# Kernel optimization log

Hardware: AMD Instinct MI355X
Metric: run time of the kernel (lower is better)

The kernel has to match this reference:

```python
import jax, jax.numpy as jnp
import numpy as np

N = 50000
E = 800000
IN_C = 128
OUT_C = 64   # per-head dim C == out_channels (concat=False)
HEADS = 4
FFN_H = 256
SQRT_HALF = 0.70710678
LN_EPS = 1e-7


def setup_inputs() -> dict:
    key = jax.random.key(0)
    ks = jax.random.split(key, 16)
    s = 0.05
    return {
        "x": jax.random.normal(ks[0], (N, IN_C), jnp.float32),
        "edge_index": jax.random.randint(ks[1], (2, E), 0, N, jnp.int64),
        # GATv2 params
        "Wl": jax.random.normal(ks[2], (HEADS * OUT_C, IN_C), jnp.float32) * s,
        "Wr": jax.random.normal(ks[3], (HEADS * OUT_C, IN_C), jnp.float32) * s,
        "att": jax.random.normal(ks[4], (HEADS, OUT_C), jnp.float32) * s,
        "bias": jax.random.normal(ks[5], (OUT_C,), jnp.float32) * s,
        # block linears
        "W_affn1": jax.random.normal(ks[6], (OUT_C, IN_C), jnp.float32) * s,
        "b_affn1": jnp.zeros((OUT_C,), jnp.float32),
        "W_affn2": jax.random.normal(ks[7], (OUT_C, OUT_C), jnp.float32) * s,
        "b_affn2": jnp.zeros((OUT_C,), jnp.float32),
        # layernorms
        "g1": jnp.ones((IN_C,), jnp.float32),
        "beta1": jnp.zeros((IN_C,), jnp.float32),
        "g2": jnp.ones((OUT_C,), jnp.float32),
        "beta2": jnp.zeros((OUT_C,), jnp.float32),
        # FFN: out_channels -> 256 -> out_channels
        "W1": jax.random.normal(ks[8], (FFN_H, OUT_C), jnp.float32) * s,
        "b1": jnp.zeros((FFN_H,), jnp.float32),
        "W2": jax.random.normal(ks[9], (OUT_C, FFN_H), jnp.float32) * s,
        "b2": jnp.zeros((OUT_C,), jnp.float32),
    }


def _ln(v, g, b):
    m = jnp.mean(v, axis=-1, keepdims=True)
    var = jnp.var(v, axis=-1, keepdims=True)
    return (v - m) * jax.lax.rsqrt(var + LN_EPS) * g + b


def reference(x, edge_index, Wl, Wr, att, bias, W_affn1, b_affn1,
              W_affn2, b_affn2, g1, beta1, g2, beta2, W1, b1, W2, b2):
    n = x.shape[0]
    H, C = att.shape
    dst = edge_index[0]
    src = edge_index[1]

    x_res = x @ W_affn1.T + b_affn1            # (N, OUT_C)
    h = _ln(x, g1, beta1)                      # (N, IN_C)

    # GATv2 attention (concat=False, no self loops)
    x_l = (h @ Wl.T).reshape(n, H, C)
    x_r = (h @ Wr.T).reshape(n, H, C)
    x_j = x_r[src]                             # (E, H, C)
    e = jax.nn.leaky_relu(x_l[dst] + x_j, 0.2) # (E, H, C)
    logits = jnp.einsum('ehc,hc->eh', e, att)  # (E, H)

    # segment softmax over destination nodes (per head)
    mx = jax.ops.segment_max(logits, dst, num_segments=n)
    ex = jnp.exp(logits - mx[dst])
    den = jax.ops.segment_sum(ex, dst, num_segments=n)
    alpha = ex / (den[dst] + 1e-16)            # (E, H)

    agg = jnp.zeros((n, H, C), x.dtype).at[dst].add(x_j * alpha[..., None])
    attn_out = jnp.mean(agg, axis=1) + bias    # (N, OUT_C)

    out = SQRT_HALF * attn_out + SQRT_HALF * x_res

    # FFN half of the block (pre-LN, matching the attention half's structure)
    h2 = _ln(out, g2, beta2)
    f = jax.nn.relu(h2 @ W1.T + b1) @ W2.T + b2
    res2 = out @ W_affn2.T + b_affn2
    return SQRT_HALF * f + SQRT_HALF * res2
```

## Files before the change

### kernel.cpp

```cpp
#include <hip/hip_runtime.h>
#include <hip/hip_bf16.h>
#include <hip/hip_fp16.h>
#include <math.h>


#define SQRT_HALF 0.70710678f
#define LN_EPS 1e-7f

typedef __attribute__((ext_vector_type(8))) short bf16x8;
typedef __attribute__((ext_vector_type(4))) float f32x4;
typedef _Float16 f16x2 __attribute__((ext_vector_type(2)));

__device__ __forceinline__ float wave_reduce_sum64(float v) {
  #pragma unroll
  for (int m = 1; m < 64; m <<= 1) v += __shfl_xor(v, m, 64);
  return v;
}
__device__ __forceinline__ unsigned short f2bf_bits(float f) {
  __hip_bfloat16 b = __float2bfloat16(f);
  return *reinterpret_cast<unsigned short*>(&b);
}
__device__ __forceinline__ unsigned int pack2bf(float lo, float hi) {
  return (unsigned int)f2bf_bits(lo) | ((unsigned int)f2bf_bits(hi) << 16);
}
__device__ __forceinline__ __half2 u2h(unsigned int u) {
  union { unsigned int u; __half2 h; } c; c.u = u; return c.h;
}
__device__ __forceinline__ __half2 h2abs(__half2 v) {
  union { __half2 h; unsigned int u; } c; c.h = v;
  c.u &= 0x7fff7fffu;
  return c.h;
}
__device__ __forceinline__ f16x2 h2f(__half2 h) {
  union { __half2 h; f16x2 f; } c; c.h = h; return c.f;
}
__device__ __forceinline__ __half2 shflx_h2(__half2 v, int m) {
  union { unsigned int u; __half2 h; } c; c.h = v;
  c.u = (unsigned int)__shfl_xor((int)c.u, m, 64);
  return c.h;
}
__device__ __forceinline__ float dpp_xor1_add(float p) {
  int t = __builtin_amdgcn_update_dpp(0, __float_as_int(p), 0xB1, 0xf, 0xf, true);
  return p + __int_as_float(t);
}
__device__ __forceinline__ float dpp_xor2_add(float p) {
  int t = __builtin_amdgcn_update_dpp(0, __float_as_int(p), 0x4E, 0xf, 0xf, true);
  return p + __int_as_float(t);
}
__device__ __forceinline__ bf16x8 cvt8(float4 a0, float4 a1) {
  bf16x8 v;
  v[0] = (short)f2bf_bits(a0.x); v[1] = (short)f2bf_bits(a0.y);
  v[2] = (short)f2bf_bits(a0.z); v[3] = (short)f2bf_bits(a0.w);
  v[4] = (short)f2bf_bits(a1.x); v[5] = (short)f2bf_bits(a1.y);
  v[6] = (short)f2bf_bits(a1.z); v[7] = (short)f2bf_bits(a1.w);
  return v;
}

#define NCHUNK 128
#define SBUK 4608

__global__ __launch_bounds__(256) void prep_kernel(
    const float* __restrict__ x, const float* __restrict__ g1,
    const float* __restrict__ beta1, __hip_bfloat16* __restrict__ h,
    const float* __restrict__ wl, const float* __restrict__ wr,
    const float* __restrict__ wa1, const float* __restrict__ w1,
    const float* __restrict__ w2, const float* __restrict__ wa2,
    const float* __restrict__ b2c, const float* __restrict__ ba2,
    const float* __restrict__ att,
    __hip_bfloat16* __restrict__ wcat, __hip_bfloat16* __restrict__ wa1b,
    __hip_bfloat16* __restrict__ w1b, __hip_bfloat16* __restrict__ w2b,
    __hip_bfloat16* __restrict__ wa2b, __half* __restrict__ att2,
    float* __restrict__ biasc,
    const int* __restrict__ ei, unsigned int* __restrict__ counts,
    int E_, int n, int NBUK, int S, int gLN) {
  __shared__ unsigned int bins[256];
  int bx = blockIdx.x, tid = threadIdx.x;
  if (bx < gLN) {
    int node = bx * 4 + (tid >> 6);
    if (node >= n) return;
    int lane = tid & 63;
    const float* xr = x + (size_t)node * 128;
    float a = xr[lane], c = xr[lane + 64];
    float s1 = wave_reduce_sum64(a + c) * (1.f / 128.f);
    float s2 = wave_reduce_sum64(a * a + c * c) * (1.f / 128.f);
    float inv = rsqrtf(s2 - s1 * s1 + LN_EPS);
    __hip_bfloat16* hr = h + (size_t)node * 128;
    hr[lane]      = __float2bfloat16((a - s1) * inv * g1[lane] + beta1[lane]);
    hr[lane + 64] =
        __float2bfloat16((c - s1) * inv * g1[lane + 64] + beta1[lane + 64]);
  } else if (bx < gLN + NCHUNK) {
    int c = bx - gLN;
    bins[tid] = 0u;
    __syncthreads();
    int e0 = c * S, e1 = c * S + S;
    if (e1 > E_) e1 = E_;
    for (int e = e0 + tid; e < e1; e += 256)
      atomicAdd(&bins[ei[e] >> 8], 1u);
    __syncthreads();
    if (tid < NBUK) counts[(size_t)c * NBUK + tid] = bins[tid];
  } else {
    int gid = (bx - gLN - NCHUNK) * 256 + tid;
    for (int i = gid; i < 110912; i += 64 * 256) {
      if (i < 65536) {
        wcat[i] = __float2bfloat16(i < 32768 ? wl[i] : wr[i - 32768]);
      } else if (i < 73728) {
        int j = i - 65536; wa1b[j] = __float2bfloat16(wa1[j]);
      } else if (i < 90112) {
        int j = i - 73728; w1b[j] = __float2bfloat16(w1[j]);
      } else if (i < 106496) {
        int j = i - 90112; w2b[j] = __float2bfloat16(w2[j]);
      } else if (i < 110592) {
        int j = i - 106496; wa2b[j] = __float2bfloat16(wa2[j]);
      } else if (i < 110848) {
        int j = i - 110592; att2[j] = __float2half(att[j]);
      } else {
        int j = i - 110848; biasc[j] = SQRT_HALF * (b2c[j] + ba2[j]);
      }
    }
  }
}

__global__ __launch_bounds__(256) void scanA_kernel(
    unsigned int* __restrict__ counts, unsigned int* __restrict__ totals,
    int NBUK) {
  int b = blockIdx.x * 4 + (threadIdx.x >> 6);
  if (b >= NBUK) return;
  int lane = threadIdx.x & 63;
  unsigned int a0 = counts[(size_t)(2 * lane) * NBUK + b];
  unsigned int a1 = counts[(size_t)(2 * lane + 1) * NBUK + b];
  unsigned int ps = a0 + a1;
  unsigned int run = ps;
  #pragma unroll
  for (int off = 1; off < 64; off <<= 1) {
    unsigned int u = __shfl_up(run, off, 64);
    if (lane >= off) run += u;
  }
  unsigned int excl = run - ps;
  counts[(size_t)(2 * lane) * NBUK + b] = excl;
  counts[(size_t)(2 * lane + 1) * NBUK + b] = excl + a0;
  if (lane == 63) totals[b] = run;
}

__global__ __launch_bounds__(256) void mfma_pre(
    const short* __restrict__ h, const float* __restrict__ x,
    const short* __restrict__ wcat, const short* __restrict__ wa1b,
    const float* __restrict__ ba1, __half* __restrict__ xlxr,
    float* __restrict__ xres, const int* __restrict__ ei,
    const unsigned int* __restrict__ counts,
    unsigned int* __restrict__ recs,
    int E_, int n, int NBUK, int S, int ntiles) {
  __shared__ unsigned int bins[256];
  int tid = threadIdx.x;
  int wv = tid >> 6, l = tid & 63;
  int lane_m = l & 15, kg = l >> 4;
  if (blockIdx.y < 4) {
    int bn = blockIdx.y * 128;
    bf16x8 wf[4][8];
    const short* wp = wcat + (size_t)(bn + lane_m) * 128 + kg * 8;
    #pragma unroll
    for (int ks = 0; ks < 4; ++ks)
      #pragma unroll
      for (int ct = 0; ct < 8; ++ct)
        wf[ks][ct] = *(const bf16x8*)(wp + (size_t)ct * 16 * 128 + ks * 32);
    for (int t = blockIdx.x; t < ntiles; t += gridDim.x) {
      int node = t * 64 + wv * 16 + lane_m;
      int nodec = node < n ? node : n - 1;
      const short* ap = h + (size_t)nodec * 128 + kg * 8;
      f32x4 acc[8] = {};
      #pragma unroll
      for (int ks = 0; ks < 4; ++ks) {
        bf16x8 af = *(const bf16x8*)(ap + ks * 32);
        #pragma unroll
        for (int ct = 0; ct < 8; ++ct)
          acc[ct] = __builtin_amdgcn_mfma_f32_16x16x32_bf16(
              wf[ks][ct], af, acc[ct], 0, 0, 0);
      }
      if (node < n) {
        #pragma unroll
        for (int ct = 0; ct < 8; ++ct) {
          int col = bn + ct * 16 + kg * 4;
          ushort4 s;
          s.x = __half_as_ushort(__float2half(acc[ct][0]));
          s.y = __half_as_ushort(__float2half(acc[ct][1]));
          s.z = __half_as_ushort(__float2half(acc[ct][2]));
          s.w = __half_as_ushort(__float2half(acc[ct][3]));
          *(ushort4*)((unsigned short*)xlxr + (size_t)node * 512 + col) = s;
        }
      }
    }
  } else if (blockIdx.y == 4) {
    bf16x8 wf[4][4];
    const short* wp = wa1b + (size_t)lane_m * 128 + kg * 8;
    #pragma unroll
    for (int ks = 0; ks < 4; ++ks)
      #pragma unroll
      for (int ct = 0; ct < 4; ++ct)
        wf[ks][ct] = *(const bf16x8*)(wp + (size_t)ct * 16 * 128 + ks * 32);
    float4 bias4[4];
    #pragma unroll
    for (int ct = 0; ct < 4; ++ct)
      bias4[ct] = *(const float4*)(ba1 + ct * 16 + kg * 4);
    for (int t = blockIdx.x; t < ntiles; t += gridDim.x) {
      int node = t * 64 + wv * 16 + lane_m;
      int nodec = node < n ? node : n - 1;
      const float* xrow = x + (size_t)nodec * 128 + kg * 8;
      bf16x8 af[4];
      #pragma unroll
      for (int ks = 0; ks < 4; ++ks) {
        float4 a0 = *(const float4*)(xrow + ks * 32);
        float4 a1 = *(const float4*)(xrow + ks * 32 + 4);
        af[ks] = cvt8(a0, a1);
      }
      f32x4 acc[4] = {};
      #pragma unroll
      for (int ks = 0; ks < 4; ++ks)
        #pragma unroll
        for (int ct = 0; ct < 4; ++ct)
          acc[ct] = __builtin_amdgcn_mfma_f32_16x16x32_bf16(
              wf[ks][ct], af[ks], acc[ct], 0, 0, 0);
      if (node < n) {
        #pragma unroll
        for (int ct = 0; ct < 4; ++ct) {
          int col = ct * 16 + kg * 4;
          *(float4*)(xres + (size_t)node * 64 + col) = make_float4(
              acc[ct][0] + ((const float*)&bias4[ct])[0],
              acc[ct][1] + ((const float*)&bias4[ct])[1],
              acc[ct][2] + ((const float*)&bias4[ct])[2],
              acc[ct][3] + ((const float*)&bias4[ct])[3]);
        }
      }
    }
  } else {
    int c = blockIdx.x;
    if (c >= NCHUNK) return;
    bins[tid] = 0u;
    __syncthreads();
    int e0 = c * S, e1 = c * S + S;
    if (e1 > E_) e1 = E_;
    const unsigned int* cpref = counts + (size_t)c * NBUK;
    for (int e = e0 + tid; e < e1; e += 256) {
      int dst = ei[e], src = ei[E_ + e];
      int b = dst >> 8;
      unsigned int pos = atomicAdd(&bins[b], 1u);
      unsigned int off = (unsigned int)b * SBUK + cpref[b] + pos;
      if (off < (unsigned int)(b + 1) * SBUK)
        recs[off] = ((unsigned int)(dst & 255) << 16) | (unsigned int)src;
    }
  }
}

__global__ __launch_bounds__(512) void bucket_kernel(
    const unsigned int* __restrict__ recs,
    const unsigned int* __restrict__ totals,
    unsigned short* __restrict__ ell, unsigned int* __restrict__ degw,
    int n) {
  __shared__ unsigned int bins[256];
  __shared__ unsigned short ellb[256 * 64];
  int b = blockIdx.x, tid = threadIdx.x;
  if (tid < 256) bins[tid] = 0u;
  __syncthreads();
  unsigned int start = (unsigned int)b * SBUK;
  unsigned int nrec = totals[b];
  for (unsigned int i = tid; i < nrec; i += 512) {
    unsigned int r = recs[start + i];
    int dlow = (int)(r >> 16);
    unsigned int pos = atomicAdd(&bins[dlow], 1u);
    if (pos < 64) ellb[(dlow << 6) + pos] = (unsigned short)(r & 0xffffu);
  }
  __syncthreads();
  if (tid < 256) {
    int d = (int)bins[tid];
    d = d < 64 ? d : 64;
    unsigned short fill = d > 0 ? ellb[(tid << 6) + d - 1] : (unsigned short)0;
    for (int s = d; s < 64; ++s) ellb[(tid << 6) + s] = fill;
  }
  __syncthreads();
  int node0 = b << 8;
  int nn = n - node0;
  nn = nn < 256 ? nn : 256;
  int nquad = nn * 16;
  ushort4* gq = (ushort4*)(ell + ((size_t)node0 << 6));
  const ushort4* lq = (const ushort4*)ellb;
  for (int qd = tid; qd < nquad; qd += 512) gq[qd] = lq[qd];
  int nw = (nn + 3) >> 2;
  for (int w = tid; w < nw; w += 512) {
    unsigned int d0 = bins[4 * w + 0], d1 = bins[4 * w + 1];
    unsigned int d2 = bins[4 * w + 2], d3 = bins[4 * w + 3];
    d0 = d0 < 64u ? d0 : 64u; d1 = d1 < 64u ? d1 : 64u;
    d2 = d2 < 64u ? d2 : 64u; d3 = d3 < 64u ? d3 : 64u;
    degw[(node0 >> 2) + w] = d0 | (d1 << 8) | (d2 << 16) | (d3 << 24);
  }
}

__global__ __launch_bounds__(256) void fused_edge_kernel(
    const unsigned int* __restrict__ degw, const unsigned short* __restrict__ ell,
    const __half* __restrict__ xlxr,
    const __half* __restrict__ att2, const float* __restrict__ xres,
    const float* __restrict__ bias, const float* __restrict__ g2,
    const float* __restrict__ b2, __hip_bfloat16* __restrict__ outb,
    __hip_bfloat16* __restrict__ h2, int n) {
  int node = blockIdx.x * 4 + (threadIdx.x >> 6);
  if (node >= n) return;
  int lane = threadIdx.x & 63;
  int half_ = lane >> 5;
  int hl = lane & 31;
  int q = hl & 7;
  int off8 = (hl >> 3) * 64 + q * 8;
  uint4 va = *(const uint4*)(xlxr + (size_t)node * 512 + off8);
  __half2 xa2[4] = {u2h(va.x), u2h(va.y), u2h(va.z), u2h(va.w)};
  uint4 vt = *(const uint4*)(att2 + off8);
  const __half2 c06 = __float2half2_rn(0.6f);
  const __half2 c04 = __float2half2_rn(0.4f);
  __half2 at6[4], at4[4];
  #pragma unroll
  for (int c = 0; c < 4; ++c) {
    __half2 a = u2h(((const unsigned int*)&vt)[c]);
    at6[c] = __hmul2(c06, a);
    at4[c] = __hmul2(c04, a);
  }
  int d = (int)((degw[node >> 2] >> ((node & 3) * 8)) & 0xffu);
  float den = 0.f;
  __half2 ac2[4] = {__float2half2_rn(0.f), __float2half2_rn(0.f),
                    __float2half2_rn(0.f), __float2half2_rn(0.f)};
  if (d > 0) {
    int dpairs = d >> 1;
    const __half* xrbase = xlxr + 256 + off8;
    int myidx = (int)ell[((size_t)node << 6) + lane];
    int srcA = __shfl(myidx, half_, 64);
    int srcB = __shfl(myidx, 2 + half_, 64);
    uint4 vbA = *(const uint4*)(xrbase + (size_t)srcA * 512);
    uint4 vbB = *(const uint4*)(xrbase + (size_t)srcB * 512);
    #pragma unroll 2
    for (int k = 0; k < dpairs; ++k) {
      int srcC = __shfl(myidx, 2 * k + 4 + half_, 64);
      uint4 vbC = *(const uint4*)(xrbase + (size_t)srcC * 512);
      __half2 xb2[4] = {u2h(vbA.x), u2h(vbA.y), u2h(vbA.z), u2h(vbA.w)};
      float p = 0.f;
      #pragma unroll
      for (int c = 0; c < 4; ++c) {
        __half2 s = __hadd2(xa2[c], xb2[c]);
        p = __builtin_amdgcn_fdot2(h2f(at6[c]), h2f(s), p, false);
        p = __builtin_amdgcn_fdot2(h2f(at4[c]), h2f(h2abs(s)), p, false);
      }
      p = dpp_xor1_add(p);
      p = dpp_xor2_add(p);
      p += __shfl_xor(p, 4, 64);
      float ex = __expf(p);
      den += ex;
      __half2 ex2 = __float2half2_rn(ex);
      #pragma unroll
      for (int c = 0; c < 4; ++c) ac2[c] = __hfma2(ex2, xb2[c], ac2[c]);
      vbA = vbB; vbB = vbC;
    }
    if (d & 1) {
      __half2 xb2[4] = {u2h(vbA.x), u2h(vbA.y), u2h(vbA.z), u2h(vbA.w)};
      float p = 0.f;
      #pragma unroll
      for (int c = 0; c < 4; ++c) {
        __half2 s = __hadd2(xa2[c], xb2[c]);
        p = __builtin_amdgcn_fdot2(h2f(at6[c]), h2f(s), p, false);
        p = __builtin_amdgcn_fdot2(h2f(at4[c]), h2f(h2abs(s)), p, false);
      }
      p = dpp_xor1_add(p);
      p = dpp_xor2_add(p);
      p += __shfl_xor(p, 4, 64);
      float ex = (half_ == 0) ? __expf(p) : 0.f;
      den += ex;
      __half2 ex2 = __float2half2_rn(ex);
      #pragma unroll
      for (int c = 0; c < 4; ++c) ac2[c] = __hfma2(ex2, xb2[c], ac2[c]);
    }
  }
  #pragma unroll
  for (int c = 0; c < 4; ++c) ac2[c] = __hadd2(ac2[c], shflx_h2(ac2[c], 32));
  den += __shfl_xor(den, 32, 64);
  float inv = 1.f / (den + 1e-16f);
  __half2 inv2 = __float2half2_rn(inv);
  #pragma unroll
  for (int c = 0; c < 4; ++c) {
    __half2 a = __hmul2(ac2[c], inv2);
    a = __hadd2(a, shflx_h2(a, 8));
    a = __hadd2(a, shflx_h2(a, 16));
    ac2[c] = a;
  }
  float acf[8];
  #pragma unroll
  for (int c = 0; c < 4; ++c) {
    acf[2 * c]     = __low2float(ac2[c]);
    acf[2 * c + 1] = __high2float(ac2[c]);
  }
  float o[8];
  {
    float4 bi0 = *(const float4*)(bias + q * 8);
    float4 bi1 = *(const float4*)(bias + q * 8 + 4);
    float4 xr0 = *(const float4*)(xres + (size_t)node * 64 + q * 8);
    float4 xr1 = *(const float4*)(xres + (size_t)node * 64 + q * 8 + 4);
    float bi[8] = {bi0.x, bi0.y, bi0.z, bi0.w, bi1.x, bi1.y, bi1.z, bi1.w};
    float xr[8] = {xr0.x, xr0.y, xr0.z, xr0.w, xr1.x, xr1.y, xr1.z, xr1.w};
    #pragma unroll
    for (int c = 0; c < 8; ++c)
      o[c] = SQRT_HALF * (acf[c] * 0.25f + bi[c] + xr[c]);
  }
  float s1 = 0.f, s2 = 0.f;
  #pragma unroll
  for (int c = 0; c < 8; ++c) { s1 += o[c]; s2 += o[c] * o[c]; }
  s1 = dpp_xor1_add(s1); s2 = dpp_xor1_add(s2);
  s1 = dpp_xor2_add(s1); s2 = dpp_xor2_add(s2);
  s1 += __shfl_xor(s1, 4, 64); s2 += __shfl_xor(s2, 4, 64);
  float mean = s1 * (1.f / 64.f);
  float var = s2 * (1.f / 64.f) - mean * mean;
  float rinv = rsqrtf(var + LN_EPS);
  if (lane < 8) {
    float4 g0 = *(const float4*)(g2 + q * 8);
    float4 g1v = *(const float4*)(g2 + q * 8 + 4);
    float4 e0 = *(const float4*)(b2 + q * 8);
    float4 e1 = *(const float4*)(b2 + q * 8 + 4);
    float gg[8] = {g0.x, g0.y, g0.z, g0.w, g1v.x, g1v.y, g1v.z, g1v.w};
    float ee[8] = {e0.x, e0.y, e0.z, e0.w, e1.x, e1.y, e1.z, e1.w};
    uint4 ov, hv;
    ov.x = pack2bf(o[0], o[1]); ov.y = pack2bf(o[2], o[3]);
    ov.z = pack2bf(o[4], o[5]); ov.w = pack2bf(o[6], o[7]);
    float t[8];
    #pragma unroll
    for (int c = 0; c < 8; ++c)
      t[c] = (o[c] - mean) * rinv * gg[c] + ee[c];
    hv.x = pack2bf(t[0], t[1]); hv.y = pack2bf(t[2], t[3]);
    hv.z = pack2bf(t[4], t[5]); hv.w = pack2bf(t[6], t[7]);
    *(uint4*)((unsigned short*)outb + (size_t)node * 64 + q * 8) = ov;
    *(uint4*)((unsigned short*)h2 + (size_t)node * 64 + q * 8) = hv;
  }
}

__global__ __launch_bounds__(256) void ffn_fused(
    const __hip_bfloat16* __restrict__ h2, const __hip_bfloat16* __restrict__ outb,
    const __hip_bfloat16* __restrict__ w1b, const __hip_bfloat16* __restrict__ w2b,
    const __hip_bfloat16* __restrict__ wa2b, const float* __restrict__ b1,
    const float* __restrict__ biasc, float* __restrict__ out,
    int n, int ntiles) {
  __shared__ unsigned short lds[4][16][280];
  int tid = threadIdx.x;
  int wv = tid >> 6, l = tid & 63;
  int lane_m = l & 15, kg = l >> 4;
  bf16x8 wf1[2][16];
  #pragma unroll
  for (int ks = 0; ks < 2; ++ks)
    #pragma unroll
    for (int ct = 0; ct < 16; ++ct)
      wf1[ks][ct] = *(const bf16x8*)(
          (const short*)w1b + (size_t)(ct * 16 + lane_m) * 64 + ks * 32 + kg * 8);
  for (int t = blockIdx.x; t < ntiles; t += gridDim.x) {
    int node = t * 64 + wv * 16 + lane_m;
    int nodec = node < n ? node : n - 1;
    const short* hp = (const short*)h2 + (size_t)nodec * 64 + kg * 8;
    bf16x8 af1[2];
    af1[0] = *(const bf16x8*)(hp);
    af1[1] = *(const bf16x8*)(hp + 32);
    f32x4 acc1[16] = {};
    #pragma unroll
    for (int ks = 0; ks < 2; ++ks)
      #pragma unroll
      for (int ct = 0; ct < 16; ++ct)
        acc1[ct] = __builtin_amdgcn_mfma_f32_16x16x32_bf16(
            wf1[ks][ct], af1[ks], acc1[ct], 0, 0, 0);
    #pragma unroll
    for (int ct = 0; ct < 16; ++ct) {
      float4 bb = *(const float4*)(b1 + ct * 16 + kg * 4);
      ushort4 s;
      s.x = f2bf_bits(fmaxf(acc1[ct][0] + bb.x, 0.f));
      s.y = f2bf_bits(fmaxf(acc1[ct][1] + bb.y, 0.f));
      s.z = f2bf_bits(fmaxf(acc1[ct][2] + bb.z, 0.f));
      s.w = f2bf_bits(fmaxf(acc1[ct][3] + bb.w, 0.f));
      *(ushort4*)&lds[wv][lane_m][ct * 16 + kg * 4] = s;
    }
    f32x4 acc2[4] = {};
    #pragma unroll
    for (int ks = 0; ks < 8; ++ks) {
      bf16x8 af2 = *(const bf16x8*)&lds[wv][lane_m][ks * 32 + kg * 8];
      #pragma unroll
      for (int ct = 0; ct < 4; ++ct) {
        bf16x8 wf2 = *(const bf16x8*)(
            (const short*)w2b + (size_t)(ct * 16 + lane_m) * 256 + ks * 32 + kg * 8);
        acc2[ct] = __builtin_amdgcn_mfma_f32_16x16x32_bf16(
            wf2, af2, acc2[ct], 0, 0, 0);
      }
    }
    const short* op = (const short*)outb + (size_t)nodec * 64 + kg * 8;
    #pragma unroll
    for (int ks = 0; ks < 2; ++ks) {
      bf16x8 afo = *(const bf16x8*)(op + ks * 32);
      #pragma unroll
      for (int ct = 0; ct < 4; ++ct) {
        bf16x8 wfo = *(const bf16x8*)(
            (const short*)wa2b + (size_t)(ct * 16 + lane_m) * 64 + ks * 32 + kg * 8);
        acc2[ct] = __builtin_amdgcn_mfma_f32_16x16x32_bf16(
            wfo, afo, acc2[ct], 0, 0, 0);
      }
    }
    if (node < n) {
      #pragma unroll
      for (int ct = 0; ct < 4; ++ct) {
        float4 bc = *(const float4*)(biasc + ct * 16 + kg * 4);
        float4 v = make_float4(SQRT_HALF * acc2[ct][0] + bc.x,
                               SQRT_HALF * acc2[ct][1] + bc.y,
                               SQRT_HALF * acc2[ct][2] + bc.z,
                               SQRT_HALF * acc2[ct][3] + bc.w);
        *(float4*)(out + (size_t)node * 64 + ct * 16 + kg * 4) = v;
      }
    }
  }
}

extern "C" void kernel_launch(void* const* d_in, const int* in_sizes, int n_in,
                              void* d_out, int out_size, void* d_ws,
                              size_t ws_size, hipStream_t stream) {
  const float* x       = (const float*)d_in[0];
  const int*   ei      = (const int*)d_in[1];
  const float* Wl      = (const float*)d_in[2];
  const float* Wr      = (const float*)d_in[3];
  const float* att     = (const float*)d_in[4];
  const float* bias    = (const float*)d_in[5];
  const float* W_affn1 = (const float*)d_in[6];
  const float* b_affn1 = (const float*)d_in[7];
  const float* W_affn2 = (const float*)d_in[8];
  const float* b_affn2 = (const float*)d_in[9];
  const float* g1      = (const float*)d_in[10];
  const float* beta1   = (const float*)d_in[11];
  const float* g2      = (const float*)d_in[12];
  const float* beta2   = (const float*)d_in[13];
  const float* W1      = (const float*)d_in[14];
  const float* b1      = (const float*)d_in[15];
  const float* W2      = (const float*)d_in[16];
  const float* b2      = (const float*)d_in[17];
  int n  = in_sizes[0] / 128;
  int E_ = in_sizes[1] / 2;

  int NBUK = (n + 255) >> 8;
  int S = (E_ + NCHUNK - 1) / NCHUNK;
  int ntiles = (n + 63) / 64;
  int gLN = (n + 3) / 4;

  float* ws = (float*)d_ws;
  size_t o_xlxr = 0;
  size_t o_h    = o_xlxr + (size_t)n * 256;
  size_t o_xres = o_h + (size_t)n * 64;
  size_t o_h2   = o_xres + (size_t)n * 64;
  size_t o_outb = o_h2 + (size_t)n * 32;
  size_t o_w    = o_outb + (size_t)n * 32;
  __half* xlxr         = (__half*)(ws + o_xlxr);
  __hip_bfloat16* h    = (__hip_bfloat16*)(ws + o_h);
  float* xres          = ws + o_xres;
  __hip_bfloat16* h2   = (__hip_bfloat16*)(ws + o_h2);
  __hip_bfloat16* outb = (__hip_bfloat16*)(ws + o_outb);
  __hip_bfloat16* wcat = (__hip_bfloat16*)(ws + o_w);
  __hip_bfloat16* wa1b = (__hip_bfloat16*)(ws + o_w + 32768);
  __hip_bfloat16* w1b  = (__hip_bfloat16*)(ws + o_w + 36864);
  __hip_bfloat16* w2b  = (__hip_bfloat16*)(ws + o_w + 45056);
  __hip_bfloat16* wa2b = (__hip_bfloat16*)(ws + o_w + 53248);
  __half* att2         = (__half*)(ws + o_w + 55296);
  float* biasc         = ws + o_w + 55424;
  size_t o_srt = o_w + 55488;
  unsigned int* counts = (unsigned int*)(ws + o_srt);
  unsigned int* totals = counts + (size_t)NCHUNK * NBUK;
  unsigned int* degw   = totals + NBUK;
  unsigned int* recs   = degw + ((n + 3) >> 2);
  unsigned short* ell  = (unsigned short*)(recs + (size_t)NBUK * SBUK);

  prep_kernel<<<gLN + NCHUNK + 64, 256, 0, stream>>>(
      x, g1, beta1, h, Wl, Wr, W_affn1, W1, W2, W_affn2, b2, b_affn2,
      att, wcat, wa1b, w1b, w2b, wa2b, att2, biasc, ei, counts,
      E_, n, NBUK, S, gLN);

  scanA_kernel<<<(NBUK + 3) / 4, 256, 0, stream>>>(counts, totals, NBUK);

  mfma_pre<<<dim3(NCHUNK, 6), 256, 0, stream>>>(
      (const short*)h, x, (const short*)wcat, (const short*)wa1b,
      b_affn1, xlxr, xres, ei, counts, recs, E_, n, NBUK, S, ntiles);

  bucket_kernel<<<NBUK, 512, 0, stream>>>(recs, totals, ell, degw, n);

  fused_edge_kernel<<<(n + 3) / 4, 256, 0, stream>>>(
      degw, ell, xlxr, att2, xres, bias, g2, beta2, outb, h2, n);

  ffn_fused<<<ntiles, 256, 0, stream>>>(
      h2, outb, w1b, w2b, wa2b, b1, biasc, (float*)d_out, n, ntiles);
}
```

Baseline: 188.3 us.

## Merge preprocessing kernels into one persistent kernel with grid-wide barriers

```diff
diff --git a/kernel.cpp b/kernel.cpp
--- a/kernel.cpp
+++ b/kernel.cpp
@@ -58,237 +58,232 @@
 
 #define NCHUNK 128
 #define SBUK 4608
-
-__global__ __launch_bounds__(256) void prep_kernel(
+#define NBLK 512
+
+__device__ __forceinline__ void gsync(unsigned int* cnt, unsigned int target) {
+  __syncthreads();
+  if (threadIdx.x == 0) {
+    __hip_atomic_fetch_add(cnt, 1u, __ATOMIC_ACQ_REL, __HIP_MEMORY_SCOPE_AGENT);
+    while (__hip_atomic_load(cnt, __ATOMIC_ACQUIRE,
+                             __HIP_MEMORY_SCOPE_AGENT) < target) {}
+  }
+  __syncthreads();
+}
+
+__global__ __launch_bounds__(256, 2) void mega_pre(
     const float* __restrict__ x, const float* __restrict__ g1,
     const float* __restrict__ beta1, __hip_bfloat16* __restrict__ h,
     const float* __restrict__ wl, const float* __restrict__ wr,
-    const float* __restrict__ wa1, const float* __restrict__ w1,
-    const float* __restrict__ w2, const float* __restrict__ wa2,
-    const float* __restrict__ b2c, const float* __restrict__ ba2,
-    const float* __restrict__ att,
+    const float* __restrict__ wa1, const float* __restrict__ ba1,
+    const float* __restrict__ w1, const float* __restrict__ w2,
+    const float* __restrict__ wa2, const float* __restrict__ b2c,
+    const float* __restrict__ ba2, const float* __restrict__ att,
     __hip_bfloat16* __restrict__ wcat, __hip_bfloat16* __restrict__ wa1b,
     __hip_bfloat16* __restrict__ w1b, __hip_bfloat16* __restrict__ w2b,
     __hip_bfloat16* __restrict__ wa2b, __half* __restrict__ att2,
     float* __restrict__ biasc,
     const int* __restrict__ ei, unsigned int* __restrict__ counts,
-    int E_, int n, int NBUK, int S, int gLN) {
+    unsigned int* __restrict__ totals, unsigned int* __restrict__ recs,
+    unsigned short* __restrict__ ell, unsigned int* __restrict__ degw,
+    __half* __restrict__ xlxr, float* __restrict__ xres,
+    unsigned int* __restrict__ barrier_,
+    int E_, int n, int NBUK, int S, int ntiles, int gLN) {
   __shared__ unsigned int bins[256];
-  int bx = blockIdx.x, tid = threadIdx.x;
-  if (bx < gLN) {
-    int node = bx * 4 + (tid >> 6);
-    if (node >= n) return;
-    int lane = tid & 63;
-    const float* xr = x + (size_t)node * 128;
-    float a = xr[lane], c = xr[lane + 64];
-    float s1 = wave_reduce_sum64(a + c) * (1.f / 128.f);
-    float s2 = wave_reduce_sum64(a * a + c * c) * (1.f / 128.f);
-    float inv = rsqrtf(s2 - s1 * s1 + LN_EPS);
-    __hip_bfloat16* hr = h + (size_t)node * 128;
-    hr[lane]      = __float2bfloat16((a - s1) * inv * g1[lane] + beta1[lane]);
-    hr[lane + 64] =
-        __float2bfloat16((c - s1) * inv * g1[lane + 64] + beta1[lane + 64]);
-  } else if (bx < gLN + NCHUNK) {
-    int c = bx - gLN;
+  int bid = blockIdx.x, tid = threadIdx.x;
+  int wv = tid >> 6, l = tid & 63;
+  int lane_m = l & 15, kg = l >> 4;
+
+  int U0 = gLN + NCHUNK + 64;
+  for (int u = bid; u < U0; u += NBLK) {
+    if (u < gLN) {
+      int node = u * 4 + wv;
+      if (node < n) {
+        const float* xr = x + (size_t)node * 128;
+        float a = xr[l], c = xr[l + 64];
+        float s1 = wave_reduce_sum64(a + c) * (1.f / 128.f);
+        float s2 = wave_reduce_sum64(a * a + c * c) * (1.f / 128.f);
+        float inv = rsqrtf(s2 - s1 * s1 + LN_EPS);
+        __hip_bfloat16* hr = h + (size_t)node * 128;
+        hr[l]      = __float2bfloat16((a - s1) * inv * g1[l] + beta1[l]);
+        hr[l + 64] =
+            __float2bfloat16((c - s1) * inv * g1[l + 64] + beta1[l + 64]);
+      }
+    } else if (u < gLN + NCHUNK) {
+      int c = u - gLN;
+      bins[tid] = 0u;
+      __syncthreads();
+      int e0 = c * S, e1 = c * S + S;
+      if (e1 > E_) e1 = E_;
+      for (int e = e0 + tid; e < e1; e += 256)
+        atomicAdd(&bins[ei[e] >> 8], 1u);
+      __syncthreads();
+      if (tid < NBUK) counts[(size_t)c * NBUK + tid] = bins[tid];
+      __syncthreads();
+    } else {
+      int gid = (u - gLN - NCHUNK) * 256 + tid;
+      for (int i = gid; i < 110912; i += 64 * 256) {
+        if (i < 65536) {
+          wcat[i] = __float2bfloat16(i < 32768 ? wl[i] : wr[i - 32768]);
+        } else if (i < 73728) {
+          int j = i - 65536; wa1b[j] = __float2bfloat16(wa1[j]);
+        } else if (i < 90112) {
+          int j = i - 73728; w1b[j] = __float2bfloat16(w1[j]);
+        } else if (i < 106496) {
+          int j = i - 90112; w2b[j] = __float2bfloat16(w2[j]);
+        } else if (i < 110592) {
+          int j = i - 106496; wa2b[j] = __float2bfloat16(wa2[j]);
+        } else if (i < 110848) {
+          int j = i - 110592; att2[j] = __float2half(att[j]);
+        } else {
+          int j = i - 110848; biasc[j] = SQRT_HALF * (b2c[j] + ba2[j]);
+        }
+      }
+    }
+  }
+  gsync(barrier_, NBLK);
+
+  int U1 = (NBUK + 3) >> 2;
+  for (int u = bid; u < U1; u += NBLK) {
+    int b = u * 4 + wv;
+    if (b < NBUK) {
+      unsigned int a0 = counts[(size_t)(2 * l) * NBUK + b];
+      unsigned int a1 = counts[(size_t)(2 * l + 1) * NBUK + b];
+      unsigned int ps = a0 + a1;
+      unsigned int run = ps;
+      #pragma unroll
+      for (int off = 1; off < 64; off <<= 1) {
+        unsigned int uu = __shfl_up(run, off, 64);
+        if (l >= off) run += uu;
+      }
+      unsigned int excl = run - ps;
+      counts[(size_t)(2 * l) * NBUK + b] = excl;
+      counts[(size_t)(2 * l + 1) * NBUK + b] = excl + a0;
+      if (l == 63) totals[b] = run;
+    }
+  }
+  gsync(barrier_, 2 * NBLK);
+
+  int U2 = NCHUNK + 5 * ntiles;
+  for (int u = bid; u < U2; u += NBLK) {
+    if (u < NCHUNK) {
+      int c = u;
+      bins[tid] = 0u;
+      __syncthreads();
+      int e0 = c * S, e1 = c * S + S;
+      if (e1 > E_) e1 = E_;
+      const unsigned int* cpref = counts + (size_t)c * NBUK;
+      for (int e = e0 + tid; e < e1; e += 256) {
+        int dst = ei[e], src = ei[E_ + e];
+        int b = dst >> 8;
+        unsigned int pos = atomicAdd(&bins[b], 1u);
+        unsigned int off = (unsigned int)b * SBUK + cpref[b] + pos;
+        if (off < (unsigned int)(b + 1) * SBUK)
+          recs[off] = ((unsigned int)(dst & 255) << 16) | (unsigned int)src;
+      }
+      __syncthreads();
+    } else {
+      int v = u - NCHUNK;
+      int s = v / ntiles;
+      int t = v - s * ntiles;
+      if (s < 4) {
+        int bn = s * 128;
+        bf16x8 wf[4][8];
+        const short* wp =
+            (const short*)wcat + (size_t)(bn + lane_m) * 128 + kg * 8;
+        #pragma unroll
+        for (int ks = 0; ks < 4; ++ks)
+          #pragma unroll
+          for (int ct = 0; ct < 8; ++ct)
+            wf[ks][ct] = *(const bf16x8*)(wp + (size_t)ct * 16 * 128 + ks * 32);
+        int node = t * 64 + wv * 16 + lane_m;
+        int nodec = node < n ? node : n - 1;
+        const short* ap = (const short*)h + (size_t)nodec * 128 + kg * 8;
+        f32x4 acc[8] = {};
+        #pragma unroll
+        for (int ks = 0; ks < 4; ++ks) {
+          bf16x8 af = *(const bf16x8*)(ap + ks * 32);
+          #pragma unroll
+          for (int ct = 0; ct < 8; ++ct)
+            acc[ct] = __builtin_amdgcn_mfma_f32_16x16x32_bf16(
+                wf[ks][ct], af, acc[ct], 0, 0, 0);
+        }
+        if (node < n) {
+          #pragma unroll
+          for (int ct = 0; ct < 8; ++ct) {
+            int col = bn + ct * 16 + kg * 4;
+            ushort4 st;
+            st.x = __half_as_ushort(__float2half(acc[ct][0]));
+            st.y = __half_as_ushort(__float2half(acc[ct][1]));
+            st.z = __half_as_ushort(__float2half(acc[ct][2]));
+            st.w = __half_as_ushort(__float2half(acc[ct][3]));
+            *(ushort4*)((unsigned short*)xlxr + (size_t)node * 512 + col) = st;
+          }
+        }
+      } else {
+        bf16x8 wf[4][4];
+        const short* wp = (const short*)wa1b + (size_t)lane_m * 128 + kg * 8;
+        #pragma unroll
+        for (int ks = 0; ks < 4; ++ks)
+          #pragma unroll
+          for (int ct = 0; ct < 4; ++ct)
+            wf[ks][ct] = *(const bf16x8*)(wp + (size_t)ct * 16 * 128 + ks * 32);
+        int node = t * 64 + wv * 16 + lane_m;
+        int nodec = node < n ? node : n - 1;
+        const float* xrow = x + (size_t)nodec * 128 + kg * 8;
+        bf16x8 af[4];
+        #pragma unroll
+        for (int ks = 0; ks < 4; ++ks) {
+          float4 a0 = *(const float4*)(xrow + ks * 32);
+          float4 a1 = *(const float4*)(xrow + ks * 32 + 4);
+          af[ks] = cvt8(a0, a1);
+        }
+        f32x4 acc[4] = {};
+        #pragma unroll
+        for (int ks = 0; ks < 4; ++ks)
+          #pragma unroll
+          for (int ct = 0; ct < 4; ++ct)
+            acc[ct] = __builtin_amdgcn_mfma_f32_16x16x32_bf16(
+                wf[ks][ct], af[ks], acc[ct], 0, 0, 0);
+        if (node < n) {
+          #pragma unroll
+          for (int ct = 0; ct < 4; ++ct) {
+            int col = ct * 16 + kg * 4;
+            float4 bb = *(const float4*)(ba1 + col);
+            *(float4*)(xres + (size_t)node * 64 + col) = make_float4(
+                acc[ct][0] + bb.x, acc[ct][1] + bb.y,
+                acc[ct][2] + bb.z, acc[ct][3] + bb.w);
+          }
+        }
+      }
+    }
+  }
+  gsync(barrier_, 3 * NBLK);
+
+  for (int b = bid; b < NBUK; b += NBLK) {
     bins[tid] = 0u;
     __syncthreads();
-    int e0 = c * S, e1 = c * S + S;
-    if (e1 > E_) e1 = E_;
-    for (int e = e0 + tid; e < e1; e += 256)
-      atomicAdd(&bins[ei[e] >> 8], 1u);
+    unsigned int start = (unsigned int)b * SBUK;
+    unsigned int nrec = totals[b];
+    int node0 = b << 8;
+    for (unsigned int i = tid; i < nrec; i += 256) {
+      unsigned int r = recs[start + i];
+      int dlow = (int)(r >> 16);
+      unsigned int pos = atomicAdd(&bins[dlow], 1u);
+      if (pos < 64)
+        ell[((size_t)(node0 + dlow) << 6) + pos] = (unsigned short)(r & 0xffffu);
+    }
     __syncthreads();
-    if (tid < NBUK) counts[(size_t)c * NBUK + tid] = bins[tid];
-  } else {
-    int gid = (bx - gLN - NCHUNK) * 256 + tid;
-    for (int i = gid; i < 110912; i += 64 * 256) {
-      if (i < 65536) {
-        wcat[i] = __float2bfloat16(i < 32768 ? wl[i] : wr[i - 32768]);
-      } else if (i < 73728) {
-        int j = i - 65536; wa1b[j] = __float2bfloat16(wa1[j]);
-      } else if (i < 90112) {
-        int j = i - 73728; w1b[j] = __float2bfloat16(w1[j]);
-      } else if (i < 106496) {
-        int j = i - 90112; w2b[j] = __float2bfloat16(w2[j]);
-      } else if (i < 110592) {
-        int j = i - 106496; wa2b[j] = __float2bfloat16(wa2[j]);
-      } else if (i < 110848) {
-        int j = i - 110592; att2[j] = __float2half(att[j]);
-      } else {
-        int j = i - 110848; biasc[j] = SQRT_HALF * (b2c[j] + ba2[j]);
-      }
-    }
-  }
-}
-
-__global__ __launch_bounds__(256) void scanA_kernel(
-    unsigned int* __restrict__ counts, unsigned int* __restrict__ totals,
-    int NBUK) {
-  int b = blockIdx.x * 4 + (threadIdx.x >> 6);
-  if (b >= NBUK) return;
-  int lane = threadIdx.x & 63;
-  unsigned int a0 = counts[(size_t)(2 * lane) * NBUK + b];
-  unsigned int a1 = counts[(size_t)(2 * lane + 1) * NBUK + b];
-  unsigned int ps = a0 + a1;
-  unsigned int run = ps;
-  #pragma unroll
-  for (int off = 1; off < 64; off <<= 1) {
-    unsigned int u = __shfl_up(run, off, 64);
-    if (lane >= off) run += u;
-  }
-  unsigned int excl = run - ps;
-  counts[(size_t)(2 * lane) * NBUK + b] = excl;
-  counts[(size_t)(2 * lane + 1) * NBUK + b] = excl + a0;
-  if (lane == 63) totals[b] = run;
-}
-
-__global__ __launch_bounds__(256) void mfma_pre(
-    const short* __restrict__ h, const float* __restrict__ x,
-    const short* __restrict__ wcat, const short* __restrict__ wa1b,
-    const float* __restrict__ ba1, __half* __restrict__ xlxr,
-    float* __restrict__ xres, const int* __restrict__ ei,
-    const unsigned int* __restrict__ counts,
-    unsigned int* __restrict__ recs,
-    int E_, int n, int NBUK, int S, int ntiles) {
-  __shared__ unsigned int bins[256];
-  int tid = threadIdx.x;
-  int wv = tid >> 6, l = tid & 63;
-  int lane_m = l & 15, kg = l >> 4;
-  if (blockIdx.y < 4) {
-    int bn = blockIdx.y * 128;
-    bf16x8 wf[4][8];
-    const short* wp = wcat + (size_t)(bn + lane_m) * 128 + kg * 8;
-    #pragma unroll
-    for (int ks = 0; ks < 4; ++ks)
-      #pragma unroll
-      for (int ct = 0; ct < 8; ++ct)
-        wf[ks][ct] = *(const bf16x8*)(wp + (size_t)ct * 16 * 128 + ks * 32);
-    for (int t = blockIdx.x; t < ntiles; t += gridDim.x) {
-      int node = t * 64 + wv * 16 + lane_m;
-      int nodec = node < n ? node : n - 1;
-      const short* ap = h + (size_t)nodec * 128 + kg * 8;
-      f32x4 acc[8] = {};
-      #pragma unroll
-      for (int ks = 0; ks < 4; ++ks) {
-        bf16x8 af = *(const bf16x8*)(ap + ks * 32);
-        #pragma unroll
-        for (int ct = 0; ct < 8; ++ct)
-          acc[ct] = __builtin_amdgcn_mfma_f32_16x16x32_bf16(
-              wf[ks][ct], af, acc[ct], 0, 0, 0);
-      }
-      if (node < n) {
-        #pragma unroll
-        for (int ct = 0; ct < 8; ++ct) {
-          int col = bn + ct * 16 + kg * 4;
-          ushort4 s;
-          s.x = __half_as_ushort(__float2half(acc[ct][0]));
-          s.y = __half_as_ushort(__float2half(acc[ct][1]));
-          s.z = __half_as_ushort(__float2half(acc[ct][2]));
-          s.w = __half_as_ushort(__float2half(acc[ct][3]));
-          *(ushort4*)((unsigned short*)xlxr + (size_t)node * 512 + col) = s;
-        }
-      }
-    }
-  } else if (blockIdx.y == 4) {
-    bf16x8 wf[4][4];
-    const short* wp = wa1b + (size_t)lane_m * 128 + kg * 8;
-    #pragma unroll
-    for (int ks = 0; ks < 4; ++ks)
-      #pragma unroll
-      for (int ct = 0; ct < 4; ++ct)
-        wf[ks][ct] = *(const bf16x8*)(wp + (size_t)ct * 16 * 128 + ks * 32);
-    float4 bias4[4];
-    #pragma unroll
-    for (int ct = 0; ct < 4; ++ct)
-      bias4[ct] = *(const float4*)(ba1 + ct * 16 + kg * 4);
-    for (int t = blockIdx.x; t < ntiles; t += gridDim.x) {
-      int node = t * 64 + wv * 16 + lane_m;
-      int nodec = node < n ? node : n - 1;
-      const float* xrow = x + (size_t)nodec * 128 + kg * 8;
-      bf16x8 af[4];
-      #pragma unroll
-      for (int ks = 0; ks < 4; ++ks) {
-        float4 a0 = *(const float4*)(xrow + ks * 32);
-        float4 a1 = *(const float4*)(xrow + ks * 32 + 4);
-        af[ks] = cvt8(a0, a1);
-      }
-      f32x4 acc[4] = {};
-      #pragma unroll
-      for (int ks = 0; ks < 4; ++ks)
-        #pragma unroll
-        for (int ct = 0; ct < 4; ++ct)
-          acc[ct] = __builtin_amdgcn_mfma_f32_16x16x32_bf16(
-              wf[ks][ct], af[ks], acc[ct], 0, 0, 0);
-      if (node < n) {
-        #pragma unroll
-        for (int ct = 0; ct < 4; ++ct) {
-          int col = ct * 16 + kg * 4;
-          *(float4*)(xres + (size_t)node * 64 + col) = make_float4(
-              acc[ct][0] + ((const float*)&bias4[ct])[0],
-              acc[ct][1] + ((const float*)&bias4[ct])[1],
-              acc[ct][2] + ((const float*)&bias4[ct])[2],
-              acc[ct][3] + ((const float*)&bias4[ct])[3]);
-        }
-      }
-    }
-  } else {
-    int c = blockIdx.x;
-    if (c >= NCHUNK) return;
-    bins[tid] = 0u;
+    int nn = n - node0;
+    nn = nn < 256 ? nn : 256;
+    int nw = (nn + 3) >> 2;
+    for (int w = tid; w < nw; w += 256) {
+      unsigned int d0 = bins[4 * w + 0], d1 = bins[4 * w + 1];
+      unsigned int d2 = bins[4 * w + 2], d3 = bins[4 * w + 3];
+      d0 = d0 < 64u ? d0 : 64u; d1 = d1 < 64u ? d1 : 64u;
+      d2 = d2 < 64u ? d2 : 64u; d3 = d3 < 64u ? d3 : 64u;
+      degw[(node0 >> 2) + w] = d0 | (d1 << 8) | (d2 << 16) | (d3 << 24);
+    }
     __syncthreads();
-    int e0 = c * S, e1 = c * S + S;
-    if (e1 > E_) e1 = E_;
-    const unsigned int* cpref = counts + (size_t)c * NBUK;
-    for (int e = e0 + tid; e < e1; e += 256) {
-      int dst = ei[e], src = ei[E_ + e];
-      int b = dst >> 8;
-      unsigned int pos = atomicAdd(&bins[b], 1u);
-      unsigned int off = (unsigned int)b * SBUK + cpref[b] + pos;
-      if (off < (unsigned int)(b + 1) * SBUK)
-        recs[off] = ((unsigned int)(dst & 255) << 16) | (unsigned int)src;
-    }
-  }
-}
-
-__global__ __launch_bounds__(512) void bucket_kernel(
-    const unsigned int* __restrict__ recs,
-    const unsigned int* __restrict__ totals,
-    unsigned short* __restrict__ ell, unsigned int* __restrict__ degw,
-    int n) {
-  __shared__ unsigned int bins[256];
-  __shared__ unsigned short ellb[256 * 64];
-  int b = blockIdx.x, tid = threadIdx.x;
-  if (tid < 256) bins[tid] = 0u;
-  __syncthreads();
-  unsigned int start = (unsigned int)b * SBUK;
-  unsigned int nrec = totals[b];
-  for (unsigned int i = tid; i < nrec; i += 512) {
-    unsigned int r = recs[start + i];
-    int dlow = (int)(r >> 16);
-    unsigned int pos = atomicAdd(&bins[dlow], 1u);
-    if (pos < 64) ellb[(dlow << 6) + pos] = (unsigned short)(r & 0xffffu);
-  }
-  __syncthreads();
-  if (tid < 256) {
-    int d = (int)bins[tid];
-    d = d < 64 ? d : 64;
-    unsigned short fill = d > 0 ? ellb[(tid << 6) + d - 1] : (unsigned short)0;
-    for (int s = d; s < 64; ++s) ellb[(tid << 6) + s] = fill;
-  }
-  __syncthreads();
-  int node0 = b << 8;
-  int nn = n - node0;
-  nn = nn < 256 ? nn : 256;
-  int nquad = nn * 16;
-  ushort4* gq = (ushort4*)(ell + ((size_t)node0 << 6));
-  const ushort4* lq = (const ushort4*)ellb;
-  for (int qd = tid; qd < nquad; qd += 512) gq[qd] = lq[qd];
-  int nw = (nn + 3) >> 2;
-  for (int w = tid; w < nw; w += 512) {
-    unsigned int d0 = bins[4 * w + 0], d1 = bins[4 * w + 1];
-    unsigned int d2 = bins[4 * w + 2], d3 = bins[4 * w + 3];
-    d0 = d0 < 64u ? d0 : 64u; d1 = d1 < 64u ? d1 : 64u;
-    d2 = d2 < 64u ? d2 : 64u; d3 = d3 < 64u ? d3 : 64u;
-    degw[(node0 >> 2) + w] = d0 | (d1 << 8) | (d2 << 16) | (d3 << 24);
   }
 }
 
@@ -319,20 +314,24 @@
     at4[c] = __hmul2(c04, a);
   }
   int d = (int)((degw[node >> 2] >> ((node & 3) * 8)) & 0xffu);
+  d = d < 64 ? d : 64;
   float den = 0.f;
   __half2 ac2[4] = {__float2half2_rn(0.f), __float2half2_rn(0.f),
                     __float2half2_rn(0.f), __float2half2_rn(0.f)};
   if (d > 0) {
+    int dm1 = d - 1;
     int dpairs = d >> 1;
     const __half* xrbase = xlxr + 256 + off8;
-    int myidx = (int)ell[((size_t)node << 6) + lane];
-    int srcA = __shfl(myidx, half_, 64);
-    int srcB = __shfl(myidx, 2 + half_, 64);
+    int myidx = (int)ell[((size_t)node << 6) + (lane <= dm1 ? lane : dm1)];
+    int srcA = __shfl(myidx, half_ <= dm1 ? half_ : dm1, 64);
+    int srcB = __shfl(myidx, 2 + half_ <= dm1 ? 2 + half_ : dm1, 64);
     uint4 vbA = *(const uint4*)(xrbase + (size_t)srcA * 512);
     uint4 vbB = *(const uint4*)(xrbase + (size_t)srcB * 512);
     #pragma unroll 2
     for (int k = 0; k < dpairs; ++k) {
-      int srcC = __shfl(myidx, 2 * k + 4 + half_, 64);
+      int jC = 2 * k + 4 + half_;
+      jC = jC <= dm1 ? jC : dm1;
+      int srcC = __shfl(myidx, jC, 64);
       uint4 vbC = *(const uint4*)(xrbase + (size_t)srcC * 512);
       __half2 xb2[4] = {u2h(vbA.x), u2h(vbA.y), u2h(vbA.z), u2h(vbA.w)};
       float p = 0.f;
@@ -559,24 +558,20 @@
   __half* att2         = (__half*)(ws + o_w + 55296);
   float* biasc         = ws + o_w + 55424;
   size_t o_srt = o_w + 55488;
-  unsigned int* counts = (unsigned int*)(ws + o_srt);
-  unsigned int* totals = counts + (size_t)NCHUNK * NBUK;
-  unsigned int* degw   = totals + NBUK;
-  unsigned int* recs   = degw + ((n + 3) >> 2);
-  unsigned short* ell  = (unsigned short*)(recs + (size_t)NBUK * SBUK);
-
-  prep_kernel<<<gLN + NCHUNK + 64, 256, 0, stream>>>(
-      x, g1, beta1, h, Wl, Wr, W_affn1, W1, W2, W_affn2, b2, b_affn2,
-      att, wcat, wa1b, w1b, w2b, wa2b, att2, biasc, ei, counts,
-      E_, n, NBUK, S, gLN);
-
-  scanA_kernel<<<(NBUK + 3) / 4, 256, 0, stream>>>(counts, totals, NBUK);
-
-  mfma_pre<<<dim3(NCHUNK, 6), 256, 0, stream>>>(
-      (const short*)h, x, (const short*)wcat, (const short*)wa1b,
-      b_affn1, xlxr, xres, ei, counts, recs, E_, n, NBUK, S, ntiles);
-
-  bucket_kernel<<<NBUK, 512, 0, stream>>>(recs, totals, ell, degw, n);
+  unsigned int* counts  = (unsigned int*)(ws + o_srt);
+  unsigned int* totals  = counts + (size_t)NCHUNK * NBUK;
+  unsigned int* degw    = totals + NBUK;
+  unsigned int* barrier_ = degw + ((n + 3) >> 2);
+  unsigned int* recs    = barrier_ + 1;
+  unsigned short* ell   = (unsigned short*)(recs + (size_t)NBUK * SBUK);
+
+  (void)hipMemsetAsync(barrier_, 0, 4, stream);
+
+  mega_pre<<<NBLK, 256, 0, stream>>>(
+      x, g1, beta1, h, Wl, Wr, W_affn1, b_affn1, W1, W2, W_affn2, b2,
+      b_affn2, att, wcat, wa1b, w1b, w2b, wa2b, att2, biasc,
+      ei, counts, totals, recs, ell, degw, xlxr, xres, barrier_,
+      E_, n, NBUK, S, ntiles, gLN);
 
   fused_edge_kernel<<<(n + 3) / 4, 256, 0, stream>>>(
       degw, ell, xlxr, att2, xres, bias, g2, beta2, outb, h2, n);
```

Result: slower. 551.3 us (+192.8%).
